# Optimization experiments

Measured on AMD Instinct MI355X. Metric: run time of the kernel, lower is better.

Reference implementation:

```python
import jax, jax.numpy as jnp
import numpy as np
from jax import lax

B, TS, N, E = 2, 12, 5000, 80000
HEADS, OUT = 4, 16
CCH, K, HOR = 64, 3, 12
EMB = HEADS * OUT  # 64
NEG_SLOPE = 0.2    # PyG GATConv leaky_relu slope


def setup_inputs():
    key = jax.random.key(0)
    ks = jax.random.split(key, 10)
    x = jax.random.normal(ks[0], (B, TS, N), jnp.float32)
    edge_index = jax.random.randint(ks[1], (2, E), 0, N, dtype=jnp.int32)
    # GATConv params: lin (in=1 -> heads*out, no bias), att_src/att_dst [heads,out], bias [heads*out]
    Wg = jax.random.normal(ks[2], (HEADS, OUT), jnp.float32) * 0.5
    a_src = jax.random.normal(ks[3], (HEADS, OUT), jnp.float32) * 0.2
    a_dst = jax.random.normal(ks[4], (HEADS, OUT), jnp.float32) * 0.2
    bg = jax.random.normal(ks[5], (EMB,), jnp.float32) * 0.02
    # temporal Conv1d(EMB -> CCH, kernel K, padding K//2)
    Wc = jax.random.normal(ks[6], (CCH, EMB, K), jnp.float32) * 0.05
    bc = jax.random.normal(ks[7], (CCH,), jnp.float32) * 0.02
    # head Linear(CCH -> HOR)
    Wh = jax.random.normal(ks[8], (HOR, CCH), jnp.float32) * 0.05
    bh = jax.random.normal(ks[9], (HOR,), jnp.float32) * 0.02
    return {"x": x, "edge_index": edge_index, "Wg": Wg, "a_src": a_src,
            "a_dst": a_dst, "bg": bg, "Wc": Wc, "bc": bc, "Wh": Wh, "bh": bh}


def _segment_attn(e, hsrc, dst):
    """Scatter-softmax over destination nodes + weighted aggregation.
    e: [E, heads] scores; hsrc: [E, heads, out] source features; dst: [E]."""
    emax = jax.ops.segment_max(e, dst, num_segments=N)            # [N, heads]
    emax = jnp.where(jnp.isfinite(emax), emax, 0.0)
    ex = jnp.exp(e - emax[dst])                                   # [E, heads]
    den = jax.ops.segment_sum(ex, dst, num_segments=N)           # [N, heads]
    alpha = ex / (den[dst] + 1e-16)
    return jax.ops.segment_sum(alpha[:, :, None] * hsrc, dst, num_segments=N)  # [N, heads, out]


def reference(x, edge_index, Wg, a_src, a_dst, bg, Wc, bc, Wh, bh):
    src, dst = edge_index[0], edge_index[1]
    # GATConv with in_channels=1: h = W * x  -> [B, Ts, N, heads, out]
    h = x[..., None, None] * Wg
    asrc = jnp.einsum('btnhd,hd->btnh', h, a_src)                 # [B,Ts,N,heads]
    adst = jnp.einsum('btnhd,hd->btnh', h, a_dst)
    e = jax.nn.leaky_relu(asrc[:, :, src] + adst[:, :, dst], NEG_SLOPE)  # [B,Ts,E,heads]
    hsrc = h[:, :, src]                                           # [B,Ts,E,heads,out]
    e2 = e.reshape(B * TS, E, HEADS)
    hs2 = hsrc.reshape(B * TS, E, HEADS, OUT)
    agg = jax.vmap(lambda ee, hh: _segment_attn(ee, hh, dst))(e2, hs2)  # [B*Ts,N,heads,out]
    Ht = agg.reshape(B, TS, N, EMB) + bg                          # concat heads + bias
    # [B,Ts,N,C] -> [B,N,C,Ts] -> [B*N, C, Ts]
    Ht = jnp.transpose(Ht, (0, 2, 3, 1)).reshape(B * N, EMB, TS)
    z = lax.conv_general_dilated(Ht, Wc, (1,), 'SAME',
                                 dimension_numbers=('NCH', 'OIH', 'NCH'))
    z = jax.nn.relu(z + bc[None, :, None]).mean(axis=-1)          # [B*N, CCH]
    y = z @ Wh.T + bh                                             # [B*N, HOR]
    return jnp.transpose(y.reshape(B, N, HOR), (0, 2, 1))         # [B, H, N]
```

## Files before the change

### kernel.cpp

```cpp
#include <hip/hip_runtime.h>
#include <math.h>

#define BB 2
#define TSS 12
#define NN 5000
#define EE 80000
#define NHEAD 4
#define NOUT 16
#define NEMB 64
#define NCCH 64
#define KW 3
#define NHOR 12
#define NBT (BB*TSS)
#define NEG 0.2f
#define CAP 64
#define NPB 4
#define XTS 32

#define OFF_CUR  0
#define OFF_CS   5008
#define OFF_CD   5012
#define OFF_WCW  5016
#define OFF_CB   5784
#define OFF_XT   6000
#define OFF_BKT  166000

#define SCAT_BLKS 313
#define TR_TASKS  30000
#define TR_BLKS   118

__device__ __forceinline__ float lrelu(float v) { return v >= 0.f ? v : NEG * v; }

__device__ __forceinline__ void wtask(int tsk, float* __restrict__ wsF,
    const float* __restrict__ Wg, const float* __restrict__ a_src,
    const float* __restrict__ a_dst, const float* __restrict__ bg,
    const float* __restrict__ Wc)
{
    if (tsk < 768) {
        int o = tsk / 12, r = tsk % 12, hd = r / 3, k = r % 3;
        float s = 0.f;
#pragma unroll
        for (int d = 0; d < NOUT; ++d)
            s += Wg[hd * NOUT + d] * Wc[(o * NEMB + hd * NOUT + d) * KW + k];
        wsF[OFF_WCW + tsk] = s;
    } else if (tsk < 960) {
        int q = tsk - 768; int o = q / 3, k = q % 3;
        float s = 0.f;
#pragma unroll
        for (int c = 0; c < NEMB; ++c)
            s += bg[c] * Wc[(o * NEMB + c) * KW + k];
        wsF[OFF_CB + q] = s;
    } else if (tsk < 968) {
        int i = tsk - 960; int h = i & 3;
        const float* av = (i < 4) ? a_src : a_dst;
        float s = 0.f;
#pragma unroll
        for (int d = 0; d < NOUT; ++d) s += Wg[h * NOUT + d] * av[h * NOUT + d];
        wsF[(i < 4 ? OFF_CS : OFF_CD) + h] = s;
    }
}

__global__ __launch_bounds__(256) void k_bucket(
    const float* __restrict__ x, const int* __restrict__ ei,
    int* __restrict__ cur, int* __restrict__ bkt,
    float* __restrict__ wsF,
    const float* __restrict__ Wg, const float* __restrict__ a_src,
    const float* __restrict__ a_dst, const float* __restrict__ bg,
    const float* __restrict__ Wc)
{
    int bid = blockIdx.x, tid = threadIdx.x;
    if (bid < SCAT_BLKS) {
        int e = bid * 256 + tid;
        if (e < EE) {
            int s = ei[e], d = ei[EE + e];
            int pos = atomicAdd(&cur[d], 1);
            if (pos < CAP) bkt[d * CAP + pos] = s;
        }
        if (bid == 0) {
            wtask(tid,       wsF, Wg, a_src, a_dst, bg, Wc);
            wtask(tid + 256, wsF, Wg, a_src, a_dst, bg, Wc);
            wtask(tid + 512, wsF, Wg, a_src, a_dst, bg, Wc);
            wtask(tid + 768, wsF, Wg, a_src, a_dst, bg, Wc);
        }
    } else {
        int idx = (bid - SCAT_BLKS) * 256 + tid;
        if (idx < TR_TASKS) {
            int n = idx / 6, q = idx % 6;
            float4 v;
            v.x = x[(4 * q + 0) * NN + n];
            v.y = x[(4 * q + 1) * NN + n];
            v.z = x[(4 * q + 2) * NN + n];
            v.w = x[(4 * q + 3) * NN + n];
            ((float4*)(wsF + OFF_XT))[n * (XTS / 4) + q] = v;
        }
    }
}

__global__ __launch_bounds__(256) void k_segfinal(
    const int* __restrict__ cur, const int* __restrict__ bkt,
    const float* __restrict__ wsF,
    const float* __restrict__ bc, const float* __restrict__ Wh,
    const float* __restrict__ bh, float* __restrict__ out)
{
    int tid = threadIdx.x;
    int u = tid >> 6, ul = tid & 63, g = ul >> 3, gl = ul & 7;
    int node = blockIdx.x * NPB + u;
    int bt0 = 3 * g;

    __shared__ float sS[NPB][NBT][NHEAD];
    __shared__ float sz[NPB][BB][NCCH];

    const float* xT = wsF + OFF_XT;
    int cnt = cur[node]; if (cnt > CAP) cnt = CAP;
    const int* brow = bkt + node * CAP;

    int idxr[8];
#pragma unroll
    for (int i = 0; i < 8; ++i) {
        int e = gl + (i << 3);
        idxr[i] = (e < cnt) ? brow[e] : 0;
    }

    float xsr[3][8];
#pragma unroll
    for (int i = 0; i < 8; ++i) {
        int e = gl + (i << 3);
        if (e < cnt) {
            const float* r = xT + idxr[i] * XTS + bt0;
            xsr[0][i] = r[0]; xsr[1][i] = r[1]; xsr[2][i] = r[2];
        }
    }
    float xdt[3];
    {
        const float* r = xT + node * XTS + bt0;
        xdt[0] = r[0]; xdt[1] = r[1]; xdt[2] = r[2];
    }

    float cc[4], qq[4];
#pragma unroll
    for (int h = 0; h < 4; ++h) { cc[h] = wsF[OFF_CS + h]; qq[h] = wsF[OFF_CD + h]; }

#pragma unroll
    for (int t = 0; t < 3; ++t) {
#pragma unroll
        for (int h = 0; h < 4; ++h) {
            float dh = qq[h] * xdt[t];
            float a = 0.f, b = 0.f;
#pragma unroll
            for (int i = 0; i < 8; ++i) {
                int e = gl + (i << 3);
                if (e < cnt) {
                    float xs = xsr[t][i];
                    float w = __expf(lrelu(cc[h] * xs + dh));
                    a += w; b += w * xs;
                }
            }
            a += __shfl_xor(a, 1); a += __shfl_xor(a, 2); a += __shfl_xor(a, 4);
            b += __shfl_xor(b, 1); b += __shfl_xor(b, 2); b += __shfl_xor(b, 4);
            if (gl == 0) sS[u][bt0 + t][h] = b / (a + 1e-16f);
        }
    }
    __syncthreads();

    int o = ul;
    float wcw[NHEAD][KW];
#pragma unroll
    for (int hd = 0; hd < NHEAD; ++hd)
#pragma unroll
        for (int k = 0; k < KW; ++k)
            wcw[hd][k] = wsF[OFF_WCW + o * (NHEAD * KW) + hd * KW + k];
    float cbk[KW];
#pragma unroll
    for (int k = 0; k < KW; ++k) cbk[k] = wsF[OFF_CB + o * KW + k];
    float bco = bc[o];
#pragma unroll
    for (int b = 0; b < BB; ++b) {
        float acc = 0.f;
#pragma unroll
        for (int t = 0; t < TSS; ++t) {
            float zt = bco;
#pragma unroll
            for (int k = 0; k < KW; ++k) {
                int tau = t + k - 1;
                if (tau >= 0 && tau < TSS) {
                    zt += cbk[k];
#pragma unroll
                    for (int hd = 0; hd < NHEAD; ++hd)
                        zt += sS[u][b * TSS + tau][hd] * wcw[hd][k];
                }
            }
            acc += fmaxf(zt, 0.f);
        }
        sz[u][b][o] = acc * (1.f / 12.f);
    }
    __syncthreads();

    if (o < NHOR) {
#pragma unroll
        for (int b = 0; b < BB; ++b) {
            float y = bh[o];
#pragma unroll
            for (int c = 0; c < NCCH; ++c) y += sz[u][b][c] * Wh[o * NCCH + c];
            out[(b * NHOR + o) * NN + node] = y;
        }
    }
}

extern "C" void kernel_launch(void* const* d_in, const int* in_sizes, int n_in,
                              void* d_out, int out_size, void* d_ws, size_t ws_size,
                              hipStream_t stream) {
    const float* x     = (const float*)d_in[0];
    const int*   ei    = (const int*)d_in[1];
    const float* Wg    = (const float*)d_in[2];
    const float* a_src = (const float*)d_in[3];
    const float* a_dst = (const float*)d_in[4];
    const float* bg    = (const float*)d_in[5];
    const float* Wc    = (const float*)d_in[6];
    const float* bc    = (const float*)d_in[7];
    const float* Wh    = (const float*)d_in[8];
    const float* bh    = (const float*)d_in[9];
    float* out = (float*)d_out;
    int*   wsI = (int*)d_ws;
    float* wsF = (float*)d_ws;

    hipMemsetAsync(wsI + OFF_CUR, 0, NN * sizeof(int), stream);
    hipLaunchKernelGGL(k_bucket, dim3(SCAT_BLKS + TR_BLKS), dim3(256), 0, stream,
                       x, ei, wsI + OFF_CUR, wsI + OFF_BKT, wsF,
                       Wg, a_src, a_dst, bg, Wc);
    hipLaunchKernelGGL(k_segfinal, dim3(NN / NPB), dim3(256), 0, stream,
                       wsI + OFF_CUR, wsI + OFF_BKT, wsF, bc, Wh, bh, out);
}
```

Baseline: 46.49 us.

## Split preprocessing, store bucket indices as u16, vectorize bucket loads

Replaces the memset and combined bucket kernel with two kernels. The first zeroes the counters, does an LDS-tiled transpose of x and computes the folded weights on extra blocks. The second does the atomic edge scatter into a bucket array of 16-bit indices. The final kernel reads each thread's eight indices with one 16-byte vector load and swaps the per-edge branches for a multiplicative mask. This cuts bucket memory traffic and branch divergence, at the cost of an extra kernel launch and unconditional gathers of possibly uninitialized slots, which are clamped to a valid node.

```diff
diff --git a/kernel.cpp b/kernel.cpp
--- a/kernel.cpp
+++ b/kernel.cpp
@@ -25,9 +25,8 @@
 #define OFF_XT   6000
 #define OFF_BKT  166000
 
-#define SCAT_BLKS 313
-#define TR_TASKS  30000
-#define TR_BLKS   118
+#define TRB 79
+#define WTB 4
 
 __device__ __forceinline__ float lrelu(float v) { return v >= 0.f ? v : NEG * v; }
 
@@ -60,44 +59,50 @@
     }
 }
 
-__global__ __launch_bounds__(256) void k_bucket(
-    const float* __restrict__ x, const int* __restrict__ ei,
-    int* __restrict__ cur, int* __restrict__ bkt,
-    float* __restrict__ wsF,
+__global__ __launch_bounds__(256) void k_pre(
+    const float* __restrict__ x, float* __restrict__ wsF, int* __restrict__ cur,
     const float* __restrict__ Wg, const float* __restrict__ a_src,
     const float* __restrict__ a_dst, const float* __restrict__ bg,
     const float* __restrict__ Wc)
 {
     int bid = blockIdx.x, tid = threadIdx.x;
-    if (bid < SCAT_BLKS) {
-        int e = bid * 256 + tid;
-        if (e < EE) {
-            int s = ei[e], d = ei[EE + e];
-            int pos = atomicAdd(&cur[d], 1);
-            if (pos < CAP) bkt[d * CAP + pos] = s;
-        }
-        if (bid == 0) {
-            wtask(tid,       wsF, Wg, a_src, a_dst, bg, Wc);
-            wtask(tid + 256, wsF, Wg, a_src, a_dst, bg, Wc);
-            wtask(tid + 512, wsF, Wg, a_src, a_dst, bg, Wc);
-            wtask(tid + 768, wsF, Wg, a_src, a_dst, bg, Wc);
+    if (bid < TRB) {
+        __shared__ float tile[64][NBT + 1];
+        int n0 = bid * 64;
+        if (tid < 64 && n0 + tid < NN) cur[n0 + tid] = 0;
+#pragma unroll
+        for (int j = 0; j < 6; ++j) {
+            int idx = tid + j * 256;
+            int row = idx >> 6, col = idx & 63;
+            if (n0 + col < NN) tile[col][row] = x[row * NN + n0 + col];
+        }
+        __syncthreads();
+#pragma unroll
+        for (int j = 0; j < 6; ++j) {
+            int idx = tid + j * 256;
+            int nn = idx / NBT, bt = idx % NBT;
+            if (n0 + nn < NN) wsF[OFF_XT + (n0 + nn) * XTS + bt] = tile[nn][bt];
         }
     } else {
-        int idx = (bid - SCAT_BLKS) * 256 + tid;
-        if (idx < TR_TASKS) {
-            int n = idx / 6, q = idx % 6;
-            float4 v;
-            v.x = x[(4 * q + 0) * NN + n];
-            v.y = x[(4 * q + 1) * NN + n];
-            v.z = x[(4 * q + 2) * NN + n];
-            v.w = x[(4 * q + 3) * NN + n];
-            ((float4*)(wsF + OFF_XT))[n * (XTS / 4) + q] = v;
-        }
+        int tsk = (bid - TRB) * 256 + tid;
+        wtask(tsk, wsF, Wg, a_src, a_dst, bg, Wc);
+    }
+}
+
+__global__ __launch_bounds__(256) void k_scat(
+    const int* __restrict__ ei, int* __restrict__ cur,
+    unsigned short* __restrict__ bkt)
+{
+    int e = blockIdx.x * 256 + threadIdx.x;
+    if (e < EE) {
+        int s = ei[e], d = ei[EE + e];
+        int pos = atomicAdd(&cur[d], 1);
+        if (pos < CAP) bkt[d * CAP + pos] = (unsigned short)s;
     }
 }
 
 __global__ __launch_bounds__(256) void k_segfinal(
-    const int* __restrict__ cur, const int* __restrict__ bkt,
+    const int* __restrict__ cur, const unsigned short* __restrict__ bkt,
     const float* __restrict__ wsF,
     const float* __restrict__ bc, const float* __restrict__ Wh,
     const float* __restrict__ bh, float* __restrict__ out)
@@ -111,24 +116,29 @@
     __shared__ float sz[NPB][BB][NCCH];
 
     const float* xT = wsF + OFF_XT;
-    int cnt = cur[node]; if (cnt > CAP) cnt = CAP;
-    const int* brow = bkt + node * CAP;
+
+    int cnt = cur[node];
+    uint4 raw = ((const uint4*)(bkt + node * CAP))[gl];
+    if (cnt > CAP) cnt = CAP;
 
     int idxr[8];
+    idxr[0] = raw.x & 0xFFFF;  idxr[1] = raw.x >> 16;
+    idxr[2] = raw.y & 0xFFFF;  idxr[3] = raw.y >> 16;
+    idxr[4] = raw.z & 0xFFFF;  idxr[5] = raw.z >> 16;
+    idxr[6] = raw.w & 0xFFFF;  idxr[7] = raw.w >> 16;
+#pragma unroll
+    for (int i = 0; i < 8; ++i) idxr[i] = min(idxr[i], NN - 1);
+
+    int slot0 = gl * 8;
+    float msk[8];
+#pragma unroll
+    for (int i = 0; i < 8; ++i) msk[i] = (slot0 + i < cnt) ? 1.f : 0.f;
+
+    float xsr[3][8];
 #pragma unroll
     for (int i = 0; i < 8; ++i) {
-        int e = gl + (i << 3);
-        idxr[i] = (e < cnt) ? brow[e] : 0;
-    }
-
-    float xsr[3][8];
-#pragma unroll
-    for (int i = 0; i < 8; ++i) {
-        int e = gl + (i << 3);
-        if (e < cnt) {
-            const float* r = xT + idxr[i] * XTS + bt0;
-            xsr[0][i] = r[0]; xsr[1][i] = r[1]; xsr[2][i] = r[2];
-        }
+        const float* r = xT + idxr[i] * XTS + bt0;
+        xsr[0][i] = r[0]; xsr[1][i] = r[1]; xsr[2][i] = r[2];
     }
     float xdt[3];
     {
@@ -148,12 +158,9 @@
             float a = 0.f, b = 0.f;
 #pragma unroll
             for (int i = 0; i < 8; ++i) {
-                int e = gl + (i << 3);
-                if (e < cnt) {
-                    float xs = xsr[t][i];
-                    float w = __expf(lrelu(cc[h] * xs + dh));
-                    a += w; b += w * xs;
-                }
+                float xs = xsr[t][i];
+                float w = __expf(lrelu(cc[h] * xs + dh)) * msk[i];
+                a += w; b += w * xs;
             }
             a += __shfl_xor(a, 1); a += __shfl_xor(a, 2); a += __shfl_xor(a, 4);
             b += __shfl_xor(b, 1); b += __shfl_xor(b, 2); b += __shfl_xor(b, 4);
@@ -222,11 +229,12 @@
     float* out = (float*)d_out;
     int*   wsI = (int*)d_ws;
     float* wsF = (float*)d_ws;
-
-    hipMemsetAsync(wsI + OFF_CUR, 0, NN * sizeof(int), stream);
-    hipLaunchKernelGGL(k_bucket, dim3(SCAT_BLKS + TR_BLKS), dim3(256), 0, stream,
-                       x, ei, wsI + OFF_CUR, wsI + OFF_BKT, wsF,
-                       Wg, a_src, a_dst, bg, Wc);
+    unsigned short* bkt = (unsigned short*)(wsI + OFF_BKT);
+
+    hipLaunchKernelGGL(k_pre, dim3(TRB + WTB), dim3(256), 0, stream,
+                       x, wsF, wsI + OFF_CUR, Wg, a_src, a_dst, bg, Wc);
+    hipLaunchKernelGGL(k_scat, dim3((EE + 255) / 256), dim3(256), 0, stream,
+                       ei, wsI + OFF_CUR, bkt);
     hipLaunchKernelGGL(k_segfinal, dim3(NN / NPB), dim3(256), 0, stream,
-                       wsI + OFF_CUR, wsI + OFF_BKT, wsF, bc, Wh, bh, out);
-}
+                       wsI + OFF_CUR, bkt, wsF, bc, Wh, bh, out);
+}
```

Result: faster. 39.10 us (-15.9%).
